# Kernel optimization log

Hardware: AMD Instinct MI355X
Metric: run time of the kernel (lower is better)

Reference implementation:

```python
import jax, jax.numpy as jnp
import numpy as np

SEQ, D, N = 8192, 1024, 4096

def setup_inputs() -> dict:
    key = jax.random.key(0)
    kx, kw, kb = jax.random.split(key, 3)
    x = jax.random.normal(kx, (SEQ, D), dtype=jnp.float32)
    W = jax.random.normal(kw, (N, D), dtype=jnp.float32) * (1.0 / np.sqrt(D))
    b = jax.random.normal(kb, (N,), dtype=jnp.float32) * 0.01
    return {"x": x, "W": W, "b": b}

def reference(x, W, b):
    # Each NEURON computes tanh(w . e + b_i); stacking over neurons and
    # over the embedding list is a single fused matmul + bias + activation.
    # out: [seq, numNeurons]
    return jnp.tanh(jnp.einsum('sd,nd->sn', x, W) + b)
```

## Files before the change

### kernel.cpp

```cpp
#include <hip/hip_runtime.h>
#include <hip/hip_fp16.h>

#define SEQ 8192
#define DIM 1024
#define NN  4096
#define KEFF 2048
#define NT   32
#define A_BYTES ((size_t)SEQ * KEFF * 2)
#define B_BYTES ((size_t)NN * DIM * 2)

using f16x8 = __attribute__((ext_vector_type(8))) _Float16;
using f16x4 = __attribute__((ext_vector_type(4))) _Float16;
using f32x4 = __attribute__((ext_vector_type(4))) float;

typedef __attribute__((address_space(1))) unsigned char as1_u8;
typedef __attribute__((address_space(3))) unsigned char as3_u8;

__device__ __forceinline__ float fast_tanh(float x) {
    float e = __expf(2.0f * x);
    return 1.0f - 2.0f / (e + 1.0f);
}

__global__ __launch_bounds__(256) void convert_kernel(
        const float* __restrict__ x, const float* __restrict__ w,
        f16x4* __restrict__ A, f16x4* __restrict__ B) {
    const int tid = threadIdx.x;
    const int b   = blockIdx.x;
    if (b < 8192) {
        const int gid = b * 256 + tid;
        const int s   = gid >> 8;
        const int c   = gid & 255;
        const float4 v = ((const float4*)x)[(size_t)s * 256 + c];
        const float f[4] = {v.x, v.y, v.z, v.w};
        f16x4 hv, lv;
#pragma unroll
        for (int e = 0; e < 4; e++) {
            const _Float16 h = (_Float16)f[e];
            hv[e] = h;
            lv[e] = (_Float16)(f[e] - (float)h);
        }
        f16x4* dst = A + (size_t)s * 512 + c;
        dst[0]   = hv;
        dst[256] = lv;
    } else {
        const int gid = (b - 8192) * 256 + tid;
        const int n   = gid >> 8;
        const int c   = gid & 255;
        const float4 v = ((const float4*)w)[(size_t)n * 256 + c];
        const float f[4] = {v.x, v.y, v.z, v.w};
        f16x4 hv;
#pragma unroll
        for (int e = 0; e < 4; e++) hv[e] = (_Float16)f[e];
        B[(size_t)n * 256 + c] = hv;
    }
}

__global__ __launch_bounds__(512, 2) void gemm_tanh_kernel(
        const _Float16* __restrict__ A,
        const _Float16* __restrict__ B,
        const float* __restrict__ bias,
        float* __restrict__ out) {
    __shared__ _Float16 lds[65536];

    const int tid  = threadIdx.x;
    const int lane = tid & 63;
    const int wave = tid >> 6;
    const int wm   = wave >> 2;
    const int wn   = wave & 3;
    const int l15  = lane & 15;
    const int lq   = lane >> 4;

    const int xcd = blockIdx.x & 7;
    const int idx = blockIdx.x >> 3;
    const int pb  = xcd * 4 + (idx & 3);
    const int qb  = idx >> 2;
    const int rowBase = pb << 8;
    const int colBase = qb << 8;

    const int sw  = l15 & 7;
    const int gk0 = ((lq)     ^ sw) << 4;
    const int gk1 = ((4 + lq) ^ sw) << 4;
    const int aOff = wm * 2048 + l15 * 128;
    const int bOff = 32768 + wn * 2048 + l15 * 128;

    const int srow = tid >> 3;
    const int sg   = (tid & 7) ^ (srow & 7);
    const unsigned ldsWave = (unsigned)wave << 10;

    const _Float16* Ag = A + (size_t)(rowBase + srow) * KEFF + sg * 8;
    const _Float16* Bg = B + (size_t)(colBase + srow) * DIM  + sg * 8;
    char* ldsc = (char*)lds;

    auto stageA = [&](int kt, int h, int d) {
        const _Float16* g = Ag + (size_t)h * 128 * KEFF + kt * 64;
        const unsigned lo = (unsigned)d * 65536u + (unsigned)h * 16384u + ldsWave;
        __builtin_amdgcn_global_load_lds((const as1_u8*)g,
                                         (as3_u8*)(ldsc + lo), 16, 0, 0);
        __builtin_amdgcn_global_load_lds((const as1_u8*)(g + (size_t)64 * KEFF),
                                         (as3_u8*)(ldsc + lo + 8192), 16, 0, 0);
    };
    auto stageB = [&](int kt, int h, int d) {
        const _Float16* g = Bg + (size_t)h * 128 * DIM + (kt & 15) * 64;
        const unsigned lo = (unsigned)d * 65536u + 32768u + (unsigned)h * 16384u + ldsWave;
        __builtin_amdgcn_global_load_lds((const as1_u8*)g,
                                         (as3_u8*)(ldsc + lo), 16, 0, 0);
        __builtin_amdgcn_global_load_lds((const as1_u8*)(g + (size_t)64 * DIM),
                                         (as3_u8*)(ldsc + lo + 8192), 16, 0, 0);
    };

    f32x4 acc[8][4] = {};
    f16x8 aH0[4][2], aH1[4][2], bN01[2][2], bN23[2][2];

    stageA(0, 0, 0); stageA(0, 1, 0); stageB(0, 0, 0); stageB(0, 1, 0);
    stageA(1, 0, 1); stageB(1, 0, 1); stageA(1, 1, 1);
    asm volatile("s_waitcnt vmcnt(6)" ::: "memory");
    __builtin_amdgcn_s_barrier();
    {
        const char* lb = ldsc;
#pragma unroll
        for (int i = 0; i < 4; ++i) {
            aH0[i][0] = *(const f16x8*)(lb + aOff + i * 4096 + gk0);
            aH0[i][1] = *(const f16x8*)(lb + aOff + i * 4096 + gk1);
        }
#pragma unroll
        for (int j = 0; j < 2; ++j) {
            bN01[j][0] = *(const f16x8*)(lb + bOff + j * 8192 + gk0);
            bN01[j][1] = *(const f16x8*)(lb + bOff + j * 8192 + gk1);
        }
    }

    for (int t = 0; t < NT; ++t) {
        const int d  = t & 1;
        const int dn = d ^ 1;
        const char* lb  = ldsc + d * 65536;
        const char* lbn = ldsc + dn * 65536;

#pragma unroll
        for (int j = 0; j < 2; ++j) {
            bN23[j][0] = *(const f16x8*)(lb + bOff + 16384 + j * 8192 + gk0);
            bN23[j][1] = *(const f16x8*)(lb + bOff + 16384 + j * 8192 + gk1);
        }
        if (t + 1 < NT) stageB(t + 1, 1, dn);
        __builtin_amdgcn_s_barrier();
        __builtin_amdgcn_s_setprio(1);
#pragma unroll
        for (int k = 0; k < 2; ++k)
#pragma unroll
            for (int i = 0; i < 4; ++i)
#pragma unroll
                for (int j = 0; j < 2; ++j)
                    acc[i][j] = __builtin_amdgcn_mfma_f32_16x16x32_f16(
                        aH0[i][k], bN01[j][k], acc[i][j], 0, 0, 0);
        __builtin_amdgcn_s_setprio(0);
        __builtin_amdgcn_s_barrier();

#pragma unroll
        for (int i = 0; i < 4; ++i) {
            aH1[i][0] = *(const f16x8*)(lb + aOff + 16384 + i * 4096 + gk0);
            aH1[i][1] = *(const f16x8*)(lb + aOff + 16384 + i * 4096 + gk1);
        }
        if (t + 2 < NT) stageA(t + 2, 0, d);
        __builtin_amdgcn_s_barrier();
        __builtin_amdgcn_s_setprio(1);
#pragma unroll
        for (int k = 0; k < 2; ++k)
#pragma unroll
            for (int i = 0; i < 4; ++i)
#pragma unroll
                for (int j = 0; j < 2; ++j)
                    acc[i][2 + j] = __builtin_amdgcn_mfma_f32_16x16x32_f16(
                        aH0[i][k], bN23[j][k], acc[i][2 + j], 0, 0, 0);
        __builtin_amdgcn_s_setprio(0);
        __builtin_amdgcn_s_barrier();

        if (t + 2 < NT) stageB(t + 2, 0, d);
        if (t + 2 < NT) {
            asm volatile("s_waitcnt vmcnt(4)" ::: "memory");
        } else if (t + 1 < NT) {
            asm volatile("s_waitcnt vmcnt(0)" ::: "memory");
        }
        __builtin_amdgcn_s_barrier();
        __builtin_amdgcn_s_setprio(1);
#pragma unroll
        for (int k = 0; k < 2; ++k)
#pragma unroll
            for (int i = 0; i < 4; ++i)
#pragma unroll
                for (int j = 0; j < 2; ++j)
                    acc[4 + i][j] = __builtin_amdgcn_mfma_f32_16x16x32_f16(
                        aH1[i][k], bN01[j][k], acc[4 + i][j], 0, 0, 0);
        __builtin_amdgcn_s_setprio(0);
        __builtin_amdgcn_s_barrier();

        if (t + 1 < NT) {
#pragma unroll
            for (int i = 0; i < 4; ++i) {
                aH0[i][0] = *(const f16x8*)(lbn + aOff + i * 4096 + gk0);
                aH0[i][1] = *(const f16x8*)(lbn + aOff + i * 4096 + gk1);
            }
#pragma unroll
            for (int j = 0; j < 2; ++j) {
                bN01[j][0] = *(const f16x8*)(lbn + bOff + j * 8192 + gk0);
                bN01[j][1] = *(const f16x8*)(lbn + bOff + j * 8192 + gk1);
            }
        }
        if (t + 2 < NT) stageA(t + 2, 1, d);
        __builtin_amdgcn_s_barrier();
        __builtin_amdgcn_s_setprio(1);
#pragma unroll
        for (int k = 0; k < 2; ++k)
#pragma unroll
            for (int i = 0; i < 4; ++i)
#pragma unroll
                for (int j = 0; j < 2; ++j)
                    acc[4 + i][2 + j] = __builtin_amdgcn_mfma_f32_16x16x32_f16(
                        aH1[i][k], bN23[j][k], acc[4 + i][2 + j], 0, 0, 0);
        __builtin_amdgcn_s_setprio(0);
        __builtin_amdgcn_s_barrier();
    }

#pragma unroll
    for (int j = 0; j < 4; ++j) {
        const int col = colBase + (j * 4 + wn) * 16 + l15;
        const float bj = bias[col];
#pragma unroll
        for (int r = 0; r < 8; ++r) {
            const size_t rb = (size_t)(rowBase + (r * 2 + wm) * 16 + lq * 4) * NN + col;
#pragma unroll
            for (int v = 0; v < 4; ++v)
                out[rb + (size_t)v * NN] = fast_tanh(acc[r][j][v] + bj);
        }
    }
}

__global__ void naive_gemm_kernel(const float* __restrict__ x,
                                  const float* __restrict__ W,
                                  const float* __restrict__ b,
                                  float* __restrict__ out) {
    __shared__ float xs[16][17], ws[16][17];
    int n = blockIdx.x * 16 + threadIdx.x;
    int m = blockIdx.y * 16 + threadIdx.y;
    float s = 0.f;
    for (int k0 = 0; k0 < DIM; k0 += 16) {
        xs[threadIdx.y][threadIdx.x] = x[(size_t)m * DIM + k0 + threadIdx.x];
        ws[threadIdx.y][threadIdx.x] =
            W[(size_t)(blockIdx.x * 16 + threadIdx.y) * DIM + k0 + threadIdx.x];
        __syncthreads();
#pragma unroll
        for (int kk = 0; kk < 16; kk++) s += xs[threadIdx.y][kk] * ws[threadIdx.x][kk];
        __syncthreads();
    }
    out[(size_t)m * NN + n] = tanhf(s + b[n]);
}

extern "C" void kernel_launch(void* const* d_in, const int* in_sizes, int n_in,
                              void* d_out, int out_size, void* d_ws, size_t ws_size,
                              hipStream_t stream) {
    const float* x = (const float*)d_in[0];
    const float* W = (const float*)d_in[1];
    const float* b = (const float*)d_in[2];
    float* out = (float*)d_out;

    const size_t need = A_BYTES + B_BYTES;
    if (ws_size < need) {
        dim3 grid(NN / 16, SEQ / 16), block(16, 16);
        naive_gemm_kernel<<<grid, block, 0, stream>>>(x, W, b, out);
        return;
    }

    _Float16* Abuf = (_Float16*)d_ws;
    _Float16* Bbuf = Abuf + (size_t)SEQ * KEFF;

    convert_kernel<<<12288, 256, 0, stream>>>(x, W, (f16x4*)Abuf, (f16x4*)Bbuf);

    gemm_tanh_kernel<<<512, 512, 0, stream>>>(Abuf, Bbuf, b, out);
}
```

Baseline: 285.9 us.

## Fuse fp32-to-fp16 split conversion into GEMM load path, drop convert kernel

Removes the separate conversion kernel and workspace buffers. The GEMM now loads fp32 x and W through registers, converts to fp16 (hi/lo split for x) in-kernel, and writes to LDS with a register-staged double buffer in place of direct global-to-LDS loads. This avoids the extra global write and read of the converted matrices and one kernel launch. In exchange it adds VGPR pressure, conversion ALU work inside the main loop, redundant per-tile conversion across blocks, and full lgkmcnt waits before each barrier.

```diff
diff --git a/kernel.cpp b/kernel.cpp
--- a/kernel.cpp
+++ b/kernel.cpp
@@ -4,60 +4,19 @@
 #define SEQ 8192
 #define DIM 1024
 #define NN  4096
-#define KEFF 2048
-#define NT   32
-#define A_BYTES ((size_t)SEQ * KEFF * 2)
-#define B_BYTES ((size_t)NN * DIM * 2)
+#define NT  32
 
 using f16x8 = __attribute__((ext_vector_type(8))) _Float16;
-using f16x4 = __attribute__((ext_vector_type(4))) _Float16;
 using f32x4 = __attribute__((ext_vector_type(4))) float;
-
-typedef __attribute__((address_space(1))) unsigned char as1_u8;
-typedef __attribute__((address_space(3))) unsigned char as3_u8;
 
 __device__ __forceinline__ float fast_tanh(float x) {
     float e = __expf(2.0f * x);
     return 1.0f - 2.0f / (e + 1.0f);
 }
 
-__global__ __launch_bounds__(256) void convert_kernel(
-        const float* __restrict__ x, const float* __restrict__ w,
-        f16x4* __restrict__ A, f16x4* __restrict__ B) {
-    const int tid = threadIdx.x;
-    const int b   = blockIdx.x;
-    if (b < 8192) {
-        const int gid = b * 256 + tid;
-        const int s   = gid >> 8;
-        const int c   = gid & 255;
-        const float4 v = ((const float4*)x)[(size_t)s * 256 + c];
-        const float f[4] = {v.x, v.y, v.z, v.w};
-        f16x4 hv, lv;
-#pragma unroll
-        for (int e = 0; e < 4; e++) {
-            const _Float16 h = (_Float16)f[e];
-            hv[e] = h;
-            lv[e] = (_Float16)(f[e] - (float)h);
-        }
-        f16x4* dst = A + (size_t)s * 512 + c;
-        dst[0]   = hv;
-        dst[256] = lv;
-    } else {
-        const int gid = (b - 8192) * 256 + tid;
-        const int n   = gid >> 8;
-        const int c   = gid & 255;
-        const float4 v = ((const float4*)w)[(size_t)n * 256 + c];
-        const float f[4] = {v.x, v.y, v.z, v.w};
-        f16x4 hv;
-#pragma unroll
-        for (int e = 0; e < 4; e++) hv[e] = (_Float16)f[e];
-        B[(size_t)n * 256 + c] = hv;
-    }
-}
-
 __global__ __launch_bounds__(512, 2) void gemm_tanh_kernel(
-        const _Float16* __restrict__ A,
-        const _Float16* __restrict__ B,
+        const float* __restrict__ x,
+        const float* __restrict__ w,
         const float* __restrict__ bias,
         float* __restrict__ out) {
     __shared__ _Float16 lds[65536];
@@ -85,100 +44,135 @@
 
     const int srow = tid >> 3;
     const int sg   = (tid & 7) ^ (srow & 7);
-    const unsigned ldsWave = (unsigned)wave << 10;
-
-    const _Float16* Ag = A + (size_t)(rowBase + srow) * KEFF + sg * 8;
-    const _Float16* Bg = B + (size_t)(colBase + srow) * DIM  + sg * 8;
+    const int scol = sg * 8;
+
     char* ldsc = (char*)lds;
-
-    auto stageA = [&](int kt, int h, int d) {
-        const _Float16* g = Ag + (size_t)h * 128 * KEFF + kt * 64;
-        const unsigned lo = (unsigned)d * 65536u + (unsigned)h * 16384u + ldsWave;
-        __builtin_amdgcn_global_load_lds((const as1_u8*)g,
-                                         (as3_u8*)(ldsc + lo), 16, 0, 0);
-        __builtin_amdgcn_global_load_lds((const as1_u8*)(g + (size_t)64 * KEFF),
-                                         (as3_u8*)(ldsc + lo + 8192), 16, 0, 0);
-    };
-    auto stageB = [&](int kt, int h, int d) {
-        const _Float16* g = Bg + (size_t)h * 128 * DIM + (kt & 15) * 64;
-        const unsigned lo = (unsigned)d * 65536u + 32768u + (unsigned)h * 16384u + ldsWave;
-        __builtin_amdgcn_global_load_lds((const as1_u8*)g,
-                                         (as3_u8*)(ldsc + lo), 16, 0, 0);
-        __builtin_amdgcn_global_load_lds((const as1_u8*)(g + (size_t)64 * DIM),
-                                         (as3_u8*)(ldsc + lo + 8192), 16, 0, 0);
-    };
+    char* wb   = ldsc + tid * 16;
+    const float* xRow = x + (size_t)(rowBase + srow) * DIM + scol;
+    const float* wRow = w + (size_t)(colBase + srow) * DIM + scol;
 
     f32x4 acc[8][4] = {};
-    f16x8 aH0[4][2], aH1[4][2], bN01[2][2], bN23[2][2];
-
-    stageA(0, 0, 0); stageA(0, 1, 0); stageB(0, 0, 0); stageB(0, 1, 0);
-    stageA(1, 0, 1); stageB(1, 0, 1); stageA(1, 1, 1);
-    asm volatile("s_waitcnt vmcnt(6)" ::: "memory");
+    float4 stg[8];
+    f16x8 aH[4][2], bN01[2][2], bN23[2][2];
+
+    auto loadStageA = [&](int s) {
+        const int rk = (s & 15) << 6;
+#pragma unroll
+        for (int c = 0; c < 4; ++c) {
+            const float* p = xRow + (size_t)(c * 64) * DIM + rk;
+            stg[2 * c]     = *(const float4*)p;
+            stg[2 * c + 1] = *(const float4*)(p + 4);
+        }
+    };
+    auto loadStageB = [&](int s) {
+        const int rk = (s & 15) << 6;
+#pragma unroll
+        for (int c = 0; c < 4; ++c) {
+            const float* p = wRow + (size_t)(c * 64) * DIM + rk;
+            stg[2 * c]     = *(const float4*)p;
+            stg[2 * c + 1] = *(const float4*)(p + 4);
+        }
+    };
+    auto writeStageA = [&](int s, int db) {
+        char* d0 = wb + db * 65536;
+        const bool lo = (s >> 4) != 0;
+#pragma unroll
+        for (int c = 0; c < 4; ++c) {
+            const float f[8] = {stg[2*c].x, stg[2*c].y, stg[2*c].z, stg[2*c].w,
+                                stg[2*c+1].x, stg[2*c+1].y, stg[2*c+1].z, stg[2*c+1].w};
+            f16x8 hv;
+            if (lo) {
+#pragma unroll
+                for (int e = 0; e < 8; ++e) {
+                    const _Float16 h = (_Float16)f[e];
+                    hv[e] = (_Float16)(f[e] - (float)h);
+                }
+            } else {
+#pragma unroll
+                for (int e = 0; e < 8; ++e) hv[e] = (_Float16)f[e];
+            }
+            *(f16x8*)(d0 + c * 8192) = hv;
+        }
+    };
+    auto writeStageB = [&](int db) {
+        char* d0 = wb + db * 65536 + 32768;
+#pragma unroll
+        for (int c = 0; c < 4; ++c) {
+            const float f[8] = {stg[2*c].x, stg[2*c].y, stg[2*c].z, stg[2*c].w,
+                                stg[2*c+1].x, stg[2*c+1].y, stg[2*c+1].z, stg[2*c+1].w};
+            f16x8 hv;
+#pragma unroll
+            for (int e = 0; e < 8; ++e) hv[e] = (_Float16)f[e];
+            *(f16x8*)(d0 + c * 8192) = hv;
+        }
+    };
+
+    loadStageA(0); writeStageA(0, 0);
+    loadStageB(0); writeStageB(0);
+    asm volatile("s_waitcnt lgkmcnt(0)" ::: "memory");
+    __builtin_amdgcn_sched_barrier(0);
     __builtin_amdgcn_s_barrier();
-    {
-        const char* lb = ldsc;
+
+    for (int t = 0; t < NT; ++t) {
+        const int d  = t & 1;
+        const int dn = d ^ 1;
+        const char* lb = ldsc + d * 65536;
+
+        if (t + 1 < NT) loadStageA(t + 1);
 #pragma unroll
         for (int i = 0; i < 4; ++i) {
-            aH0[i][0] = *(const f16x8*)(lb + aOff + i * 4096 + gk0);
-            aH0[i][1] = *(const f16x8*)(lb + aOff + i * 4096 + gk1);
+            aH[i][0] = *(const f16x8*)(lb + aOff + i * 4096 + gk0);
+            aH[i][1] = *(const f16x8*)(lb + aOff + i * 4096 + gk1);
         }
 #pragma unroll
         for (int j = 0; j < 2; ++j) {
             bN01[j][0] = *(const f16x8*)(lb + bOff + j * 8192 + gk0);
             bN01[j][1] = *(const f16x8*)(lb + bOff + j * 8192 + gk1);
         }
-    }
-
-    for (int t = 0; t < NT; ++t) {
-        const int d  = t & 1;
-        const int dn = d ^ 1;
-        const char* lb  = ldsc + d * 65536;
-        const char* lbn = ldsc + dn * 65536;
-
+        asm volatile("s_waitcnt lgkmcnt(0)" ::: "memory");
+        __builtin_amdgcn_sched_barrier(0);
+        __builtin_amdgcn_s_barrier();
+        __builtin_amdgcn_s_setprio(1);
+#pragma unroll
+        for (int k = 0; k < 2; ++k)
+#pragma unroll
+            for (int i = 0; i < 4; ++i)
+#pragma unroll
+                for (int j = 0; j < 2; ++j)
+                    acc[i][j] = __builtin_amdgcn_mfma_f32_16x16x32_f16(
+                        aH[i][k], bN01[j][k], acc[i][j], 0, 0, 0);
+        __builtin_amdgcn_s_setprio(0);
+        __builtin_amdgcn_s_barrier();
+
+        if (t + 1 < NT) writeStageA(t + 1, dn);
 #pragma unroll
         for (int j = 0; j < 2; ++j) {
             bN23[j][0] = *(const f16x8*)(lb + bOff + 16384 + j * 8192 + gk0);
             bN23[j][1] = *(const f16x8*)(lb + bOff + 16384 + j * 8192 + gk1);
         }
-        if (t + 1 < NT) stageB(t + 1, 1, dn);
-        __builtin_amdgcn_s_barrier();
-        __builtin_amdgcn_s_setprio(1);
-#pragma unroll
-        for (int k = 0; k < 2; ++k)
-#pragma unroll
-            for (int i = 0; i < 4; ++i)
-#pragma unroll
-                for (int j = 0; j < 2; ++j)
-                    acc[i][j] = __builtin_amdgcn_mfma_f32_16x16x32_f16(
-                        aH0[i][k], bN01[j][k], acc[i][j], 0, 0, 0);
-        __builtin_amdgcn_s_setprio(0);
-        __builtin_amdgcn_s_barrier();
-
+        asm volatile("s_waitcnt lgkmcnt(0)" ::: "memory");
+        __builtin_amdgcn_sched_barrier(0);
+        __builtin_amdgcn_s_barrier();
+        __builtin_amdgcn_s_setprio(1);
+#pragma unroll
+        for (int k = 0; k < 2; ++k)
+#pragma unroll
+            for (int i = 0; i < 4; ++i)
+#pragma unroll
+                for (int j = 0; j < 2; ++j)
+                    acc[i][2 + j] = __builtin_amdgcn_mfma_f32_16x16x32_f16(
+                        aH[i][k], bN23[j][k], acc[i][2 + j], 0, 0, 0);
+        __builtin_amdgcn_s_setprio(0);
+        __builtin_amdgcn_s_barrier();
+
+        if (t + 1 < NT) loadStageB(t + 1);
 #pragma unroll
         for (int i = 0; i < 4; ++i) {
-            aH1[i][0] = *(const f16x8*)(lb + aOff + 16384 + i * 4096 + gk0);
-            aH1[i][1] = *(const f16x8*)(lb + aOff + 16384 + i * 4096 + gk1);
-        }
-        if (t + 2 < NT) stageA(t + 2, 0, d);
-        __builtin_amdgcn_s_barrier();
-        __builtin_amdgcn_s_setprio(1);
-#pragma unroll
-        for (int k = 0; k < 2; ++k)
-#pragma unroll
-            for (int i = 0; i < 4; ++i)
-#pragma unroll
-                for (int j = 0; j < 2; ++j)
-                    acc[i][2 + j] = __builtin_amdgcn_mfma_f32_16x16x32_f16(
-                        aH0[i][k], bN23[j][k], acc[i][2 + j], 0, 0, 0);
-        __builtin_amdgcn_s_setprio(0);
-        __builtin_amdgcn_s_barrier();
-
-        if (t + 2 < NT) stageB(t + 2, 0, d);
-        if (t + 2 < NT) {
-            asm volatile("s_waitcnt vmcnt(4)" ::: "memory");
-        } else if (t + 1 < NT) {
-            asm volatile("s_waitcnt vmcnt(0)" ::: "memory");
-        }
+            aH[i][0] = *(const f16x8*)(lb + aOff + 16384 + i * 4096 + gk0);
+            aH[i][1] = *(const f16x8*)(lb + aOff + 16384 + i * 4096 + gk1);
+        }
+        asm volatile("s_waitcnt lgkmcnt(0)" ::: "memory");
+        __builtin_amdgcn_sched_barrier(0);
         __builtin_amdgcn_s_barrier();
         __builtin_amdgcn_s_setprio(1);
 #pragma unroll
@@ -188,23 +182,13 @@
 #pragma unroll
                 for (int j = 0; j < 2; ++j)
                     acc[4 + i][j] = __builtin_amdgcn_mfma_f32_16x16x32_f16(
-                        aH1[i][k], bN01[j][k], acc[4 + i][j], 0, 0, 0);
-        __builtin_amdgcn_s_setprio(0);
-        __builtin_amdgcn_s_barrier();
-
-        if (t + 1 < NT) {
-#pragma unroll
-            for (int i = 0; i < 4; ++i) {
-                aH0[i][0] = *(const f16x8*)(lbn + aOff + i * 4096 + gk0);
-                aH0[i][1] = *(const f16x8*)(lbn + aOff + i * 4096 + gk1);
-            }
-#pragma unroll
-            for (int j = 0; j < 2; ++j) {
-                bN01[j][0] = *(const f16x8*)(lbn + bOff + j * 8192 + gk0);
-                bN01[j][1] = *(const f16x8*)(lbn + bOff + j * 8192 + gk1);
-            }
-        }
-        if (t + 2 < NT) stageA(t + 2, 1, d);
+                        aH[i][k], bN01[j][k], acc[4 + i][j], 0, 0, 0);
+        __builtin_amdgcn_s_setprio(0);
+        __builtin_amdgcn_s_barrier();
+
+        if (t + 1 < NT) writeStageB(dn);
+        asm volatile("s_waitcnt lgkmcnt(0)" ::: "memory");
+        __builtin_amdgcn_sched_barrier(0);
         __builtin_amdgcn_s_barrier();
         __builtin_amdgcn_s_setprio(1);
 #pragma unroll
@@ -214,7 +198,7 @@
 #pragma unroll
                 for (int j = 0; j < 2; ++j)
                     acc[4 + i][2 + j] = __builtin_amdgcn_mfma_f32_16x16x32_f16(
-                        aH1[i][k], bN23[j][k], acc[4 + i][2 + j], 0, 0, 0);
+                        aH[i][k], bN23[j][k], acc[4 + i][2 + j], 0, 0, 0);
         __builtin_amdgcn_s_setprio(0);
         __builtin_amdgcn_s_barrier();
     }
@@ -231,26 +215,6 @@
                 out[rb + (size_t)v * NN] = fast_tanh(acc[r][j][v] + bj);
         }
     }
-}
-
-__global__ void naive_gemm_kernel(const float* __restrict__ x,
-                                  const float* __restrict__ W,
-                                  const float* __restrict__ b,
-                                  float* __restrict__ out) {
-    __shared__ float xs[16][17], ws[16][17];
-    int n = blockIdx.x * 16 + threadIdx.x;
-    int m = blockIdx.y * 16 + threadIdx.y;
-    float s = 0.f;
-    for (int k0 = 0; k0 < DIM; k0 += 16) {
-        xs[threadIdx.y][threadIdx.x] = x[(size_t)m * DIM + k0 + threadIdx.x];
-        ws[threadIdx.y][threadIdx.x] =
-            W[(size_t)(blockIdx.x * 16 + threadIdx.y) * DIM + k0 + threadIdx.x];
-        __syncthreads();
-#pragma unroll
-        for (int kk = 0; kk < 16; kk++) s += xs[threadIdx.y][kk] * ws[threadIdx.x][kk];
-        __syncthreads();
-    }
-    out[(size_t)m * NN + n] = tanhf(s + b[n]);
 }
 
 extern "C" void kernel_launch(void* const* d_in, const int* in_sizes, int n_in,
@@ -260,18 +224,7 @@
     const float* W = (const float*)d_in[1];
     const float* b = (const float*)d_in[2];
     float* out = (float*)d_out;
-
-    const size_t need = A_BYTES + B_BYTES;
-    if (ws_size < need) {
-        dim3 grid(NN / 16, SEQ / 16), block(16, 16);
-        naive_gemm_kernel<<<grid, block, 0, stream>>>(x, W, b, out);
-        return;
-    }
-
-    _Float16* Abuf = (_Float16*)d_ws;
-    _Float16* Bbuf = Abuf + (size_t)SEQ * KEFF;
-
-    convert_kernel<<<12288, 256, 0, stream>>>(x, W, (f16x4*)Abuf, (f16x4*)Bbuf);
-
-    gemm_tanh_kernel<<<512, 512, 0, stream>>>(Abuf, Bbuf, b, out);
+    (void)d_ws; (void)ws_size;
+
+    gemm_tanh_kernel<<<512, 512, 0, stream>>>(x, W, b, out);
 }
```

Result: slower. 386.5 us (+35.2%).

## Switch GEMM to 256x128 tiles with triple-buffered K=32 LDS pipeline

Applied to the files above, without the earlier changes.

Replaces the 256x256 tile, 8-wave block with a 256x128 tile, 4-wave block over 1024 workgroups. It uses a three-slot LDS ring of K=32 steps, so there is one barrier per step instead of many. The XCD-aware block mapping now spreads column tiles across XCDs instead of row tiles. The aim is less barrier overhead and better occupancy, at the cost of lower arithmetic intensity per tile and more reloading of A.

```diff
diff --git a/kernel.cpp b/kernel.cpp
--- a/kernel.cpp
+++ b/kernel.cpp
@@ -5,7 +5,7 @@
 #define DIM 1024
 #define NN  4096
 #define KEFF 2048
-#define NT   32
+#define NKT 64
 #define A_BYTES ((size_t)SEQ * KEFF * 2)
 #define B_BYTES ((size_t)NN * DIM * 2)
 
@@ -55,180 +55,110 @@
     }
 }
 
-__global__ __launch_bounds__(512, 2) void gemm_tanh_kernel(
+__global__ __launch_bounds__(256, 2) void gemm_tanh_kernel(
         const _Float16* __restrict__ A,
         const _Float16* __restrict__ B,
         const float* __restrict__ bias,
         float* __restrict__ out) {
-    __shared__ _Float16 lds[65536];
+    __shared__ _Float16 lds[36864];
 
     const int tid  = threadIdx.x;
     const int lane = tid & 63;
     const int wave = tid >> 6;
-    const int wm   = wave >> 2;
-    const int wn   = wave & 3;
+    const int wm   = wave >> 1;
+    const int wn   = wave & 1;
     const int l15  = lane & 15;
     const int lq   = lane >> 4;
 
     const int xcd = blockIdx.x & 7;
     const int idx = blockIdx.x >> 3;
-    const int pb  = xcd * 4 + (idx & 3);
-    const int qb  = idx >> 2;
+    const int qb  = xcd * 4 + (idx & 3);
+    const int pb  = idx >> 2;
     const int rowBase = pb << 8;
-    const int colBase = qb << 8;
-
-    const int sw  = l15 & 7;
-    const int gk0 = ((lq)     ^ sw) << 4;
-    const int gk1 = ((4 + lq) ^ sw) << 4;
-    const int aOff = wm * 2048 + l15 * 128;
-    const int bOff = 32768 + wn * 2048 + l15 * 128;
-
-    const int srow = tid >> 3;
-    const int sg   = (tid & 7) ^ (srow & 7);
-    const unsigned ldsWave = (unsigned)wave << 10;
-
-    const _Float16* Ag = A + (size_t)(rowBase + srow) * KEFF + sg * 8;
-    const _Float16* Bg = B + (size_t)(colBase + srow) * DIM  + sg * 8;
+    const int colBase = qb << 7;
+
+    const int gsw = (lq ^ (l15 & 3)) << 4;
+    const int aFr = wm * 8192 + l15 * 64 + gsw;
+    const int bFr = 16384 + wn * 4096 + l15 * 64 + gsw;
+
+    const int srA = tid >> 2;
+    const int sgr = (tid & 3) ^ (srA & 3);
     char* ldsc = (char*)lds;
 
-    auto stageA = [&](int kt, int h, int d) {
-        const _Float16* g = Ag + (size_t)h * 128 * KEFF + kt * 64;
-        const unsigned lo = (unsigned)d * 65536u + (unsigned)h * 16384u + ldsWave;
-        __builtin_amdgcn_global_load_lds((const as1_u8*)g,
-                                         (as3_u8*)(ldsc + lo), 16, 0, 0);
-        __builtin_amdgcn_global_load_lds((const as1_u8*)(g + (size_t)64 * KEFF),
-                                         (as3_u8*)(ldsc + lo + 8192), 16, 0, 0);
+    const _Float16* Abase = A + (size_t)(rowBase + srA) * KEFF + sgr * 8;
+    const _Float16* Bbase = B + (size_t)(colBase + srA) * DIM + sgr * 8;
+
+    auto stageKT = [&](int kt, unsigned bufOff) {
+        const _Float16* ga = Abase + kt * 32;
+#pragma unroll
+        for (int i = 0; i < 4; ++i)
+            __builtin_amdgcn_global_load_lds(
+                (const as1_u8*)(ga + (size_t)i * 64 * KEFF),
+                (as3_u8*)(ldsc + bufOff + i * 4096 + tid * 16), 16, 0, 0);
+        const _Float16* gb = Bbase + (kt & 31) * 32;
+#pragma unroll
+        for (int i = 0; i < 2; ++i)
+            __builtin_amdgcn_global_load_lds(
+                (const as1_u8*)(gb + (size_t)i * 64 * DIM),
+                (as3_u8*)(ldsc + bufOff + 16384 + i * 4096 + tid * 16), 16, 0, 0);
     };
-    auto stageB = [&](int kt, int h, int d) {
-        const _Float16* g = Bg + (size_t)h * 128 * DIM + (kt & 15) * 64;
-        const unsigned lo = (unsigned)d * 65536u + 32768u + (unsigned)h * 16384u + ldsWave;
-        __builtin_amdgcn_global_load_lds((const as1_u8*)g,
-                                         (as3_u8*)(ldsc + lo), 16, 0, 0);
-        __builtin_amdgcn_global_load_lds((const as1_u8*)(g + (size_t)64 * DIM),
-                                         (as3_u8*)(ldsc + lo + 8192), 16, 0, 0);
-    };
 
     f32x4 acc[8][4] = {};
-    f16x8 aH0[4][2], aH1[4][2], bN01[2][2], bN23[2][2];
-
-    stageA(0, 0, 0); stageA(0, 1, 0); stageB(0, 0, 0); stageB(0, 1, 0);
-    stageA(1, 0, 1); stageB(1, 0, 1); stageA(1, 1, 1);
+    f16x8 aF[8], bF[4];
+
+    unsigned o0 = 0, o1 = 24576, o2 = 49152;
+
+    stageKT(0, o0);
+    stageKT(1, o1);
     asm volatile("s_waitcnt vmcnt(6)" ::: "memory");
     __builtin_amdgcn_s_barrier();
-    {
-        const char* lb = ldsc;
-#pragma unroll
-        for (int i = 0; i < 4; ++i) {
-            aH0[i][0] = *(const f16x8*)(lb + aOff + i * 4096 + gk0);
-            aH0[i][1] = *(const f16x8*)(lb + aOff + i * 4096 + gk1);
-        }
-#pragma unroll
-        for (int j = 0; j < 2; ++j) {
-            bN01[j][0] = *(const f16x8*)(lb + bOff + j * 8192 + gk0);
-            bN01[j][1] = *(const f16x8*)(lb + bOff + j * 8192 + gk1);
-        }
-    }
-
-    for (int t = 0; t < NT; ++t) {
-        const int d  = t & 1;
-        const int dn = d ^ 1;
-        const char* lb  = ldsc + d * 65536;
-        const char* lbn = ldsc + dn * 65536;
-
-#pragma unroll
-        for (int j = 0; j < 2; ++j) {
-            bN23[j][0] = *(const f16x8*)(lb + bOff + 16384 + j * 8192 + gk0);
-            bN23[j][1] = *(const f16x8*)(lb + bOff + 16384 + j * 8192 + gk1);
-        }
-        if (t + 1 < NT) stageB(t + 1, 1, dn);
-        __builtin_amdgcn_s_barrier();
+
+    for (int t = 0; t < NKT; ++t) {
+        const char* lb = ldsc + o0;
+#pragma unroll
+        for (int m = 0; m < 4; ++m) aF[m] = *(const f16x8*)(lb + aFr + m * 1024);
+#pragma unroll
+        for (int n = 0; n < 4; ++n) bF[n] = *(const f16x8*)(lb + bFr + n * 1024);
+        if (t + 2 < NKT) stageKT(t + 2, o2);
         __builtin_amdgcn_s_setprio(1);
 #pragma unroll
-        for (int k = 0; k < 2; ++k)
-#pragma unroll
-            for (int i = 0; i < 4; ++i)
-#pragma unroll
-                for (int j = 0; j < 2; ++j)
-                    acc[i][j] = __builtin_amdgcn_mfma_f32_16x16x32_f16(
-                        aH0[i][k], bN01[j][k], acc[i][j], 0, 0, 0);
+        for (int m = 0; m < 4; ++m)
+#pragma unroll
+            for (int n = 0; n < 4; ++n)
+                acc[m][n] = __builtin_amdgcn_mfma_f32_16x16x32_f16(
+                    aF[m], bF[n], acc[m][n], 0, 0, 0);
         __builtin_amdgcn_s_setprio(0);
-        __builtin_amdgcn_s_barrier();
-
-#pragma unroll
-        for (int i = 0; i < 4; ++i) {
-            aH1[i][0] = *(const f16x8*)(lb + aOff + 16384 + i * 4096 + gk0);
-            aH1[i][1] = *(const f16x8*)(lb + aOff + 16384 + i * 4096 + gk1);
-        }
-        if (t + 2 < NT) stageA(t + 2, 0, d);
-        __builtin_amdgcn_s_barrier();
+
+#pragma unroll
+        for (int m = 0; m < 4; ++m) aF[4 + m] = *(const f16x8*)(lb + aFr + (4 + m) * 1024);
         __builtin_amdgcn_s_setprio(1);
 #pragma unroll
-        for (int k = 0; k < 2; ++k)
-#pragma unroll
-            for (int i = 0; i < 4; ++i)
-#pragma unroll
-                for (int j = 0; j < 2; ++j)
-                    acc[i][2 + j] = __builtin_amdgcn_mfma_f32_16x16x32_f16(
-                        aH0[i][k], bN23[j][k], acc[i][2 + j], 0, 0, 0);
+        for (int m = 0; m < 4; ++m)
+#pragma unroll
+            for (int n = 0; n < 4; ++n)
+                acc[4 + m][n] = __builtin_amdgcn_mfma_f32_16x16x32_f16(
+                    aF[4 + m], bF[n], acc[4 + m][n], 0, 0, 0);
         __builtin_amdgcn_s_setprio(0);
-        __builtin_amdgcn_s_barrier();
-
-        if (t + 2 < NT) stageB(t + 2, 0, d);
-        if (t + 2 < NT) {
-            asm volatile("s_waitcnt vmcnt(4)" ::: "memory");
-        } else if (t + 1 < NT) {
+
+        if (t + 2 < NKT) {
+            asm volatile("s_waitcnt vmcnt(6)" ::: "memory");
+        } else if (t + 1 < NKT) {
             asm volatile("s_waitcnt vmcnt(0)" ::: "memory");
         }
         __builtin_amdgcn_s_barrier();
-        __builtin_amdgcn_s_setprio(1);
-#pragma unroll
-        for (int k = 0; k < 2; ++k)
-#pragma unroll
-            for (int i = 0; i < 4; ++i)
-#pragma unroll
-                for (int j = 0; j < 2; ++j)
-                    acc[4 + i][j] = __builtin_amdgcn_mfma_f32_16x16x32_f16(
-                        aH1[i][k], bN01[j][k], acc[4 + i][j], 0, 0, 0);
-        __builtin_amdgcn_s_setprio(0);
-        __builtin_amdgcn_s_barrier();
-
-        if (t + 1 < NT) {
-#pragma unroll
-            for (int i = 0; i < 4; ++i) {
-                aH0[i][0] = *(const f16x8*)(lbn + aOff + i * 4096 + gk0);
-                aH0[i][1] = *(const f16x8*)(lbn + aOff + i * 4096 + gk1);
-            }
-#pragma unroll
-            for (int j = 0; j < 2; ++j) {
-                bN01[j][0] = *(const f16x8*)(lbn + bOff + j * 8192 + gk0);
-                bN01[j][1] = *(const f16x8*)(lbn + bOff + j * 8192 + gk1);
-            }
-        }
-        if (t + 2 < NT) stageA(t + 2, 1, d);
-        __builtin_amdgcn_s_barrier();
-        __builtin_amdgcn_s_setprio(1);
-#pragma unroll
-        for (int k = 0; k < 2; ++k)
-#pragma unroll
-            for (int i = 0; i < 4; ++i)
-#pragma unroll
-                for (int j = 0; j < 2; ++j)
-                    acc[4 + i][2 + j] = __builtin_amdgcn_mfma_f32_16x16x32_f16(
-                        aH1[i][k], bN23[j][k], acc[4 + i][2 + j], 0, 0, 0);
-        __builtin_amdgcn_s_setprio(0);
-        __builtin_amdgcn_s_barrier();
-    }
-
-#pragma unroll
-    for (int j = 0; j < 4; ++j) {
-        const int col = colBase + (j * 4 + wn) * 16 + l15;
+        const unsigned tmp = o0; o0 = o1; o1 = o2; o2 = tmp;
+    }
+
+#pragma unroll
+    for (int n = 0; n < 4; ++n) {
+        const int col = colBase + wn * 64 + n * 16 + l15;
         const float bj = bias[col];
 #pragma unroll
-        for (int r = 0; r < 8; ++r) {
-            const size_t rb = (size_t)(rowBase + (r * 2 + wm) * 16 + lq * 4) * NN + col;
+        for (int m = 0; m < 8; ++m) {
+            const size_t rb = (size_t)(rowBase + wm * 128 + m * 16 + lq * 4) * NN + col;
 #pragma unroll
             for (int v = 0; v < 4; ++v)
-                out[rb + (size_t)v * NN] = fast_tanh(acc[r][j][v] + bj);
+                out[rb + (size_t)v * NN] = fast_tanh(acc[m][n][v] + bj);
         }
     }
 }
@@ -273,5 +203,5 @@
 
     convert_kernel<<<12288, 256, 0, stream>>>(x, W, (f16x4*)Abuf, (f16x4*)Bbuf);
 
-    gemm_tanh_kernel<<<512, 512, 0, stream>>>(Abuf, Bbuf, b, out);
-}
+    gemm_tanh_kernel<<<1024, 256, 0, stream>>>(Abuf, Bbuf, b, out);
+}
```

After: 302.7 us. 5.9% more time.

## Simplify GEMM pipeline to one-barrier double buffering with full-tile prefetch

Applied to the files above, without the earlier changes.

Replaces the finely interleaved two-stage-ahead prefetch with eight barriers per iteration by a simpler scheme. All A and B loads for the next k-tile are issued at the start of each iteration, and a single vmcnt(0)/lgkmcnt(0) wait plus barrier sits mid-iteration. It also changes the block-to-tile mapping to a column-major order grouped by XCD and relaxes launch bounds to one block per CU. The intent is to cut barrier overhead, at the risk of exposing more global-load latency because prefetch depth drops from two tiles to one.

```diff
diff --git a/kernel.cpp b/kernel.cpp
--- a/kernel.cpp
+++ b/kernel.cpp
@@ -55,7 +55,7 @@
     }
 }
 
-__global__ __launch_bounds__(512, 2) void gemm_tanh_kernel(
+__global__ __launch_bounds__(512, 1) void gemm_tanh_kernel(
         const _Float16* __restrict__ A,
         const _Float16* __restrict__ B,
         const float* __restrict__ bias,
@@ -70,10 +70,9 @@
     const int l15  = lane & 15;
     const int lq   = lane >> 4;
 
-    const int xcd = blockIdx.x & 7;
-    const int idx = blockIdx.x >> 3;
-    const int pb  = xcd * 4 + (idx & 3);
-    const int qb  = idx >> 2;
+    const int wgid = ((blockIdx.x & 7) << 6) | (blockIdx.x >> 3);
+    const int qb = wgid >> 5;
+    const int pb = wgid & 31;
     const int rowBase = pb << 8;
     const int colBase = qb << 8;
 
@@ -112,21 +111,19 @@
     f16x8 aH0[4][2], aH1[4][2], bN01[2][2], bN23[2][2];
 
     stageA(0, 0, 0); stageA(0, 1, 0); stageB(0, 0, 0); stageB(0, 1, 0);
-    stageA(1, 0, 1); stageB(1, 0, 1); stageA(1, 1, 1);
-    asm volatile("s_waitcnt vmcnt(6)" ::: "memory");
+    asm volatile("s_waitcnt vmcnt(0)" ::: "memory");
+    __builtin_amdgcn_sched_barrier(0);
     __builtin_amdgcn_s_barrier();
-    {
-        const char* lb = ldsc;
-#pragma unroll
-        for (int i = 0; i < 4; ++i) {
-            aH0[i][0] = *(const f16x8*)(lb + aOff + i * 4096 + gk0);
-            aH0[i][1] = *(const f16x8*)(lb + aOff + i * 4096 + gk1);
-        }
-#pragma unroll
-        for (int j = 0; j < 2; ++j) {
-            bN01[j][0] = *(const f16x8*)(lb + bOff + j * 8192 + gk0);
-            bN01[j][1] = *(const f16x8*)(lb + bOff + j * 8192 + gk1);
-        }
+    __builtin_amdgcn_sched_barrier(0);
+#pragma unroll
+    for (int i = 0; i < 4; ++i) {
+        aH0[i][0] = *(const f16x8*)(ldsc + aOff + i * 4096 + gk0);
+        aH0[i][1] = *(const f16x8*)(ldsc + aOff + i * 4096 + gk1);
+    }
+#pragma unroll
+    for (int j = 0; j < 2; ++j) {
+        bN01[j][0] = *(const f16x8*)(ldsc + bOff + j * 8192 + gk0);
+        bN01[j][1] = *(const f16x8*)(ldsc + bOff + j * 8192 + gk1);
     }
 
     for (int t = 0; t < NT; ++t) {
@@ -135,13 +132,16 @@
         const char* lb  = ldsc + d * 65536;
         const char* lbn = ldsc + dn * 65536;
 
+        if (t + 1 < NT) {
+            stageA(t + 1, 0, dn); stageA(t + 1, 1, dn);
+            stageB(t + 1, 0, dn); stageB(t + 1, 1, dn);
+        }
+
 #pragma unroll
         for (int j = 0; j < 2; ++j) {
             bN23[j][0] = *(const f16x8*)(lb + bOff + 16384 + j * 8192 + gk0);
             bN23[j][1] = *(const f16x8*)(lb + bOff + 16384 + j * 8192 + gk1);
         }
-        if (t + 1 < NT) stageB(t + 1, 1, dn);
-        __builtin_amdgcn_s_barrier();
         __builtin_amdgcn_s_setprio(1);
 #pragma unroll
         for (int k = 0; k < 2; ++k)
@@ -152,15 +152,12 @@
                     acc[i][j] = __builtin_amdgcn_mfma_f32_16x16x32_f16(
                         aH0[i][k], bN01[j][k], acc[i][j], 0, 0, 0);
         __builtin_amdgcn_s_setprio(0);
-        __builtin_amdgcn_s_barrier();
 
 #pragma unroll
         for (int i = 0; i < 4; ++i) {
             aH1[i][0] = *(const f16x8*)(lb + aOff + 16384 + i * 4096 + gk0);
             aH1[i][1] = *(const f16x8*)(lb + aOff + 16384 + i * 4096 + gk1);
         }
-        if (t + 2 < NT) stageA(t + 2, 0, d);
-        __builtin_amdgcn_s_barrier();
         __builtin_amdgcn_s_setprio(1);
 #pragma unroll
         for (int k = 0; k < 2; ++k)
@@ -171,26 +168,13 @@
                     acc[i][2 + j] = __builtin_amdgcn_mfma_f32_16x16x32_f16(
                         aH0[i][k], bN23[j][k], acc[i][2 + j], 0, 0, 0);
         __builtin_amdgcn_s_setprio(0);
+
+        asm volatile("s_waitcnt lgkmcnt(0)" ::: "memory");
+        __builtin_amdgcn_sched_barrier(0);
+        asm volatile("s_waitcnt vmcnt(0)" ::: "memory");
+        __builtin_amdgcn_sched_barrier(0);
         __builtin_amdgcn_s_barrier();
-
-        if (t + 2 < NT) stageB(t + 2, 0, d);
-        if (t + 2 < NT) {
-            asm volatile("s_waitcnt vmcnt(4)" ::: "memory");
-        } else if (t + 1 < NT) {
-            asm volatile("s_waitcnt vmcnt(0)" ::: "memory");
-        }
-        __builtin_amdgcn_s_barrier();
-        __builtin_amdgcn_s_setprio(1);
-#pragma unroll
-        for (int k = 0; k < 2; ++k)
-#pragma unroll
-            for (int i = 0; i < 4; ++i)
-#pragma unroll
-                for (int j = 0; j < 2; ++j)
-                    acc[4 + i][j] = __builtin_amdgcn_mfma_f32_16x16x32_f16(
-                        aH1[i][k], bN01[j][k], acc[4 + i][j], 0, 0, 0);
-        __builtin_amdgcn_s_setprio(0);
-        __builtin_amdgcn_s_barrier();
+        __builtin_amdgcn_sched_barrier(0);
 
         if (t + 1 < NT) {
 #pragma unroll
@@ -198,14 +182,25 @@
                 aH0[i][0] = *(const f16x8*)(lbn + aOff + i * 4096 + gk0);
                 aH0[i][1] = *(const f16x8*)(lbn + aOff + i * 4096 + gk1);
             }
+        }
+        __builtin_amdgcn_s_setprio(1);
+#pragma unroll
+        for (int k = 0; k < 2; ++k)
+#pragma unroll
+            for (int i = 0; i < 4; ++i)
+#pragma unroll
+                for (int j = 0; j < 2; ++j)
+                    acc[4 + i][j] = __builtin_amdgcn_mfma_f32_16x16x32_f16(
+                        aH1[i][k], bN01[j][k], acc[4 + i][j], 0, 0, 0);
+        __builtin_amdgcn_s_setprio(0);
+
+        if (t + 1 < NT) {
 #pragma unroll
             for (int j = 0; j < 2; ++j) {
                 bN01[j][0] = *(const f16x8*)(lbn + bOff + j * 8192 + gk0);
                 bN01[j][1] = *(const f16x8*)(lbn + bOff + j * 8192 + gk1);
             }
         }
-        if (t + 2 < NT) stageA(t + 2, 1, d);
-        __builtin_amdgcn_s_barrier();
         __builtin_amdgcn_s_setprio(1);
 #pragma unroll
         for (int k = 0; k < 2; ++k)
@@ -216,7 +211,6 @@
                     acc[4 + i][2 + j] = __builtin_amdgcn_mfma_f32_16x16x32_f16(
                         aH1[i][k], bN23[j][k], acc[4 + i][2 + j], 0, 0, 0);
         __builtin_amdgcn_s_setprio(0);
-        __builtin_amdgcn_s_barrier();
     }
 
 #pragma unroll
```

Result: faster. 280.2 us (-2.0%).
